# Optimization experiments

Measured on AMD Instinct MI355X. Metric: run time of the kernel, lower is better.

The kernel has to match this reference:

```python
import jax, jax.numpy as jnp
import numpy as np

B, S, D_IN = 2, 2048, 1024
H, D_HEAD = 16, 64  # n_heads, output_dim == hidden_size


def setup_inputs() -> dict:
    key = jax.random.key(0)
    k1, k2, k3 = jax.random.split(key, 3)
    x = jax.random.normal(k1, (B, S, D_IN), dtype=jnp.float32)
    # he_normal-ish init: std = sqrt(2 / fan_in)
    kernel = jax.random.normal(k2, (3, H, D_IN, D_HEAD), dtype=jnp.float32) * np.float32(np.sqrt(2.0 / D_IN))
    WO = jax.random.normal(k3, (1, H * D_HEAD, D_IN), dtype=jnp.float32) * np.float32(np.sqrt(2.0 / (H * D_HEAD)))
    return {"x": x, "kernel": kernel, "WO": WO}


def reference(x, kernel, WO):
    b, s, _ = x.shape
    h, d = kernel.shape[1], kernel.shape[3]
    # K.dot(x, kernel[i]): contract x last axis with kernel axis -2 -> (B,S,H,d);
    # original then permutes to (B,H,S,d); fuse both into one einsum.
    q = jnp.einsum('bsm,hmd->bhsd', x, kernel[0])
    k = jnp.einsum('bsm,hmd->bhsd', x, kernel[1])
    v = jnp.einsum('bsm,hmd->bhsd', x, kernel[2])
    # scores scaled by /output_dim /hidden_size /n_heads (output_dim==hidden_size)
    scale = jnp.float32(1.0 / (d * d * h))
    scores = jnp.einsum('bhsd,bhtd->bhst', q, k) * scale  # (B,H,S,S)
    attn = jax.nn.softmax(scores, axis=-1)
    out = jnp.einsum('bhst,bhtd->bhsd', attn, v)          # (B,H,S,d)
    # original: permute to (B,S,d,H) then reshape to (B,S,d*H) -> d-major, H-minor
    out = jnp.transpose(out, (0, 2, 3, 1)).reshape(b, s, d * h)
    out = jnp.einsum('bsf,fm->bsm', out, WO[0])           # (B,S,D_IN)
    return out
```

## Files before the change

### kernel.cpp

```cpp
#include <hip/hip_runtime.h>
#include <hip/hip_bf16.h>


typedef unsigned short u16;
typedef __attribute__((ext_vector_type(8))) short bf16x8;
typedef __attribute__((ext_vector_type(4))) short bf16x4;
typedef __attribute__((ext_vector_type(4))) float f32x4;
typedef __attribute__((ext_vector_type(4))) unsigned short u16x4;
typedef __attribute__((ext_vector_type(8))) unsigned short u16x8;

#define SCALE 1.52587890625e-05f

__device__ __forceinline__ u16 f2bf(float f) {
  unsigned int u = __float_as_uint(f);
  return (u16)((u + 0x7FFFu + ((u >> 16) & 1u)) >> 16);
}
__device__ __forceinline__ float bf2f(u16 v) {
  return __uint_as_float(((unsigned int)v) << 16);
}

__device__ __forceinline__ f32x4 mfma16(bf16x8 a, bf16x8 b, f32x4 c) {
  return __builtin_amdgcn_mfma_f32_16x16x32_bf16(a, b, c, 0, 0, 0);
}

__device__ __forceinline__ void gl_lds16(const u16* g, u16* l) {
  __builtin_amdgcn_global_load_lds((const __attribute__((address_space(1))) void*)g,
                                   (__attribute__((address_space(3))) void*)l, 16, 0, 0);
}

__global__ void split_f32(const float* __restrict__ x, u16* __restrict__ hi,
                          u16* __restrict__ lo, int n4) {
  int i = blockIdx.x * 256 + threadIdx.x;
  if (i >= n4) return;
  float4 v = ((const float4*)x)[i];
  float vv[4] = {v.x, v.y, v.z, v.w};
  u16x4 h, l;
#pragma unroll
  for (int j = 0; j < 4; ++j) {
    u16 hb = f2bf(vv[j]);
    h[j] = hb;
    l[j] = f2bf(vv[j] - bf2f(hb));
  }
  ((u16x4*)hi)[i] = h;
  ((u16x4*)lo)[i] = l;
}

__global__ void prep_w(const float* __restrict__ w, u16* __restrict__ bhi,
                       u16* __restrict__ blo) {
  __shared__ float t[64 * 65];
  int mt = blockIdx.x, th = blockIdx.y;
  float scl = (th < 16) ? SCALE : 1.0f;
  int tid = threadIdx.x;
  for (int i = 0; i < 16; ++i) {
    int idx = tid + i * 256;
    int ms = idx >> 6, d = idx & 63;
    t[d * 65 + ms] = w[(size_t)(th * 1024 + mt * 64 + ms) * 64 + d];
  }
  __syncthreads();
  for (int i = 0; i < 16; ++i) {
    int idx = tid + i * 256;
    int ds = idx >> 6, mm = idx & 63;
    float v = t[ds * 65 + mm] * scl;
    size_t o = (size_t)(th * 64 + ds) * 1024 + mt * 64 + mm;
    u16 hb = f2bf(v);
    bhi[o] = hb;
    blo[o] = f2bf(v - bf2f(hb));
  }
}

__global__ void prep_wo(const float* __restrict__ wo, u16* __restrict__ bhi,
                        u16* __restrict__ blo) {
  __shared__ float t[64 * 65];
  int mt = blockIdx.x, kt = blockIdx.y;
  int tid = threadIdx.x;
  for (int i = 0; i < 16; ++i) {
    int idx = tid + i * 256;
    int d = idx >> 6, mm = idx & 63;
    t[mm * 65 + d] = wo[(size_t)(d * 16 + kt) * 1024 + mt * 64 + mm];
  }
  __syncthreads();
  for (int i = 0; i < 16; ++i) {
    int idx = tid + i * 256;
    int mr = idx >> 6, dc = idx & 63;
    float v = t[mr * 65 + dc];
    size_t o = (size_t)(mt * 64 + mr) * 1024 + kt * 64 + dc;
    u16 hb = f2bf(v);
    bhi[o] = hb;
    blo[o] = f2bf(v - bf2f(hb));
  }
}

template <int MODE>
__global__ __launch_bounds__(256, 2) void gemm_split(
    const u16* __restrict__ Ah_g, const u16* __restrict__ Al_g,
    const u16* __restrict__ Bh_g, const u16* __restrict__ Bl_g,
    u16* __restrict__ Qb, u16* __restrict__ Kb, u16* __restrict__ Vb,
    float* __restrict__ Cf) {
  __shared__ __align__(16) u16 Ah[128 * 32];
  __shared__ __align__(16) u16 Al[128 * 32];
  __shared__ __align__(16) u16 Bh[128 * 32];
  __shared__ __align__(16) u16 Bl[128 * 32];
  int tid = threadIdx.x;
  int lane = tid & 63;
  int l15 = lane & 15, g = lane >> 4;
  int wv = tid >> 6, wm = wv >> 1, wn = wv & 1;
  int m0 = blockIdx.x * 128, n0 = blockIdx.y * 128;

  f32x4 acc[4][4];
#pragma unroll
  for (int i = 0; i < 4; ++i)
#pragma unroll
    for (int j = 0; j < 4; ++j) acc[i][j] = (f32x4){0.f, 0.f, 0.f, 0.f};

  int c0 = tid, c1 = tid + 256;
  int r0 = c0 >> 2, o0 = (c0 & 3) * 8;
  int r1 = c1 >> 2, o1 = (c1 & 3) * 8;
  int wb0 = (tid & 192) * 8, wb1 = ((tid & 192) + 256) * 8;

  for (int kk = 0; kk < 32; ++kk) {
    int k0 = kk * 32;
    __syncthreads();
    gl_lds16(Ah_g + (size_t)(m0 + r0) * 1024 + k0 + o0, &Ah[wb0]);
    gl_lds16(Ah_g + (size_t)(m0 + r1) * 1024 + k0 + o1, &Ah[wb1]);
    gl_lds16(Al_g + (size_t)(m0 + r0) * 1024 + k0 + o0, &Al[wb0]);
    gl_lds16(Al_g + (size_t)(m0 + r1) * 1024 + k0 + o1, &Al[wb1]);
    gl_lds16(Bh_g + (size_t)(n0 + r0) * 1024 + k0 + o0, &Bh[wb0]);
    gl_lds16(Bh_g + (size_t)(n0 + r1) * 1024 + k0 + o1, &Bh[wb1]);
    gl_lds16(Bl_g + (size_t)(n0 + r0) * 1024 + k0 + o0, &Bl[wb0]);
    gl_lds16(Bl_g + (size_t)(n0 + r1) * 1024 + k0 + o1, &Bl[wb1]);
    __syncthreads();

    bf16x8 fa_h[4], fa_l[4], fb_h[4], fb_l[4];
#pragma unroll
    for (int mi = 0; mi < 4; ++mi) {
      int off = (wm * 64 + mi * 16 + l15) * 64 + g * 16;
      fa_h[mi] = *(const bf16x8*)((const char*)Ah + off);
      fa_l[mi] = *(const bf16x8*)((const char*)Al + off);
    }
#pragma unroll
    for (int ni = 0; ni < 4; ++ni) {
      int off = (wn * 64 + ni * 16 + l15) * 64 + g * 16;
      fb_h[ni] = *(const bf16x8*)((const char*)Bh + off);
      fb_l[ni] = *(const bf16x8*)((const char*)Bl + off);
    }
#pragma unroll
    for (int mi = 0; mi < 4; ++mi)
#pragma unroll
      for (int ni = 0; ni < 4; ++ni) {
        acc[mi][ni] = mfma16(fa_h[mi], fb_h[ni], acc[mi][ni]);
        acc[mi][ni] = mfma16(fa_h[mi], fb_l[ni], acc[mi][ni]);
        acc[mi][ni] = mfma16(fa_l[mi], fb_h[ni], acc[mi][ni]);
      }
  }

#pragma unroll
  for (int mi = 0; mi < 4; ++mi)
#pragma unroll
    for (int ni = 0; ni < 4; ++ni)
#pragma unroll
      for (int r = 0; r < 4; ++r) {
        int m = m0 + wm * 64 + mi * 16 + g * 4 + r;
        int n = n0 + wn * 64 + ni * 16 + l15;
        float v = acc[mi][ni][r];
        if (MODE == 0) {
          int th = n >> 6, d = n & 63;
          int t = th >> 4, h = th & 15;
          int b = m >> 11, s = m & 2047;
          if (t == 0)
            Qb[(size_t)((b * 16 + h) * 2048 + s) * 64 + d] = f2bf(v);
          else if (t == 1)
            Kb[(size_t)((b * 16 + h) * 2048 + s) * 64 + d] = f2bf(v);
          else
            Vb[(size_t)((b * 16 + h) * 64 + d) * 2048 + s] = f2bf(v);
        } else {
          Cf[(size_t)m * 1024 + n] = v;
        }
      }
}

__global__ void colsum_v(const u16* __restrict__ Vt, float* __restrict__ cs) {
  int bh = blockIdx.x, tid = threadIdx.x;
  int d = tid >> 2, q = tid & 3;
  const u16x8* row = (const u16x8*)(Vt + (size_t)(bh * 64 + d) * 2048 + q * 512);
  float s = 0.f;
  for (int i = 0; i < 64; ++i) {
    u16x8 v = row[i];
#pragma unroll
    for (int j = 0; j < 8; ++j) s += bf2f(v[j]);
  }
  s += __shfl_xor(s, 1);
  s += __shfl_xor(s, 2);
  if (q == 0) cs[bh * 64 + d] = s;
}

__global__ __launch_bounds__(256, 2) void attn(
    const u16* __restrict__ Qb, const u16* __restrict__ Kb,
    const u16* __restrict__ Vt, const float* __restrict__ csum,
    u16* __restrict__ AOhi, u16* __restrict__ AOlo) {
  __shared__ __align__(16) u16 Kl[2][128 * 64];
  __shared__ __align__(16) u16 Vl[2][64 * 128];
  int swz = (blockIdx.x & 7) * 64 + (blockIdx.x >> 3);
  int qt = swz & 15, bh = swz >> 4;
  int tid = threadIdx.x, lane = tid & 63, w = tid >> 6;
  int l15 = lane & 15, g = lane >> 4;
  const u16* Qg = Qb + (size_t)bh * 2048 * 64;
  const u16* Kg = Kb + (size_t)bh * 2048 * 64;
  const u16* Vg = Vt + (size_t)bh * 64 * 2048;
  int q_base = qt * 128 + w * 32;
  int wbase = tid & 192;

  bf16x8 qf[2][2];
#pragma unroll
  for (int q2 = 0; q2 < 2; ++q2)
#pragma unroll
    for (int ds = 0; ds < 2; ++ds)
      qf[q2][ds] = *(const bf16x8*)(Qg + (size_t)(q_base + q2 * 16 + l15) * 64 +
                                    ds * 32 + g * 8);

  f32x4 acc_e[2][4];
#pragma unroll
  for (int i = 0; i < 4; ++i) {
    acc_e[0][i] = (f32x4){0.f, 0.f, 0.f, 0.f};
    acc_e[1][i] = (f32x4){0.f, 0.f, 0.f, 0.f};
  }
  float lsum[2] = {0.f, 0.f};

  auto STAGE = [&](int buf, int tt0) {
    int t0 = tt0 * 128;
#pragma unroll
    for (int i = 0; i < 4; ++i) {
      int c = tid + i * 256;
      int krow = c >> 3, kblk = c & 7;
      gl_lds16(Kg + (size_t)(t0 + krow) * 64 + ((kblk ^ (krow & 7)) * 8),
               &Kl[buf][(wbase + i * 256) * 8]);
      int vd = c >> 4, vsb = c & 15;
      gl_lds16(Vg + (size_t)vd * 2048 + t0 + ((vsb ^ (vd & 7)) * 8),
               &Vl[buf][(wbase + i * 256) * 8]);
    }
  };

  STAGE(0, 0);

  for (int tt0 = 0; tt0 < 16; ++tt0) {
    int cur = tt0 & 1;
    __syncthreads();
    if (tt0 + 1 < 16) STAGE(cur ^ 1, tt0 + 1);

    const char* Kc = (const char*)&Kl[cur][0];
    const char* Vc = (const char*)&Vl[cur][0];

    f32x4 sc[2][8];
#pragma unroll
    for (int tt = 0; tt < 8; ++tt) {
      sc[0][tt] = (f32x4){0.f, 0.f, 0.f, 0.f};
      sc[1][tt] = (f32x4){0.f, 0.f, 0.f, 0.f};
    }
#pragma unroll
    for (int tt = 0; tt < 8; ++tt)
#pragma unroll
      for (int ds = 0; ds < 2; ++ds) {
        int row = tt * 16 + l15;
        int off = row * 128 + ((((ds * 4 + g) ^ (row & 7)) << 4));
        bf16x8 kf = *(const bf16x8*)(Kc + off);
        sc[0][tt] = mfma16(kf, qf[0][ds], sc[0][tt]);
        sc[1][tt] = mfma16(kf, qf[1][ds], sc[1][tt]);
      }

    bf16x8 pe[2][4];
#pragma unroll
    for (int q2 = 0; q2 < 2; ++q2)
#pragma unroll
      for (int ks = 0; ks < 4; ++ks)
#pragma unroll
        for (int blk = 0; blk < 2; ++blk)
#pragma unroll
          for (int r = 0; r < 4; ++r) {
            float e = __expf(sc[q2][ks * 2 + blk][r]) - 1.0f;
            lsum[q2] += e;
            pe[q2][ks][blk * 4 + r] = (short)(__float_as_uint(e) >> 16);
          }

    int xm = (l15 & 7) << 4;
    const char* Vrow = Vc + l15 * 256;
#pragma unroll
    for (int ks = 0; ks < 4; ++ks) {
      int t0a = (ks * 64 + 8 * g) ^ xm;
      int t1a = (ks * 64 + 32 + 8 * g) ^ xm;
#pragma unroll
      for (int dt = 0; dt < 4; ++dt) {
        bf16x4 lo = *(const bf16x4*)(Vrow + dt * 4096 + t0a);
        bf16x4 hi = *(const bf16x4*)(Vrow + dt * 4096 + t1a);
        bf16x8 vf = (bf16x8){lo[0], lo[1], lo[2], lo[3],
                             hi[0], hi[1], hi[2], hi[3]};
        acc_e[0][dt] = mfma16(pe[0][ks], vf, acc_e[0][dt]);
        acc_e[1][dt] = mfma16(pe[1][ks], vf, acc_e[1][dt]);
      }
    }
  }

  float lt[2];
#pragma unroll
  for (int q2 = 0; q2 < 2; ++q2) {
    float v = lsum[q2];
    v += __shfl_xor(v, 16);
    v += __shfl_xor(v, 32);
    lt[q2] = 2048.0f + v;
  }
  float linv[2][4];
#pragma unroll
  for (int q2 = 0; q2 < 2; ++q2)
#pragma unroll
    for (int r = 0; r < 4; ++r) linv[q2][r] = 1.0f / __shfl(lt[q2], g * 4 + r);

  int b = bh >> 4, h = bh & 15;
#pragma unroll
  for (int q2 = 0; q2 < 2; ++q2)
#pragma unroll
    for (int dt = 0; dt < 4; ++dt) {
      float cv = csum[bh * 64 + dt * 16 + l15];
#pragma unroll
      for (int r = 0; r < 4; ++r) {
        int s = q_base + q2 * 16 + g * 4 + r;
        int d = dt * 16 + l15;
        float o = (cv + acc_e[q2][dt][r]) * linv[q2][r];
        u16 hv = f2bf(o);
        size_t ao = ((size_t)(b * 2048 + s) * 16 + h) * 64 + d;
        AOhi[ao] = hv;
        AOlo[ao] = f2bf(o - bf2f(hv));
      }
    }
}

extern "C" void kernel_launch(void* const* d_in, const int* in_sizes, int n_in,
                              void* d_out, int out_size, void* d_ws,
                              size_t ws_size, hipStream_t stream) {
  const float* x = (const float*)d_in[0];
  const float* krn = (const float*)d_in[1];
  const float* wo = (const float*)d_in[2];
  float* out = (float*)d_out;

  u16* p = (u16*)d_ws;
  u16* Xhi = p;   p += 4096 * 1024;
  u16* Xlo = p;   p += 4096 * 1024;
  u16* Wthi = p;  p += 3072 * 1024;
  u16* Wtlo = p;  p += 3072 * 1024;
  u16* WOthi = p; p += 1024 * 1024;
  u16* WOtlo = p; p += 1024 * 1024;
  u16* Qb = p;    p += 4194304;
  u16* Kb = p;    p += 4194304;
  u16* Vtb = p;   p += 4194304;
  u16* AOhi = p;  p += 4194304;
  u16* AOlo = p;  p += 4194304;
  float* Csum = (float*)p;

  split_f32<<<4096, 256, 0, stream>>>(x, Xhi, Xlo, 1048576);
  prep_w<<<dim3(16, 48), 256, 0, stream>>>(krn, Wthi, Wtlo);
  prep_wo<<<dim3(16, 16), 256, 0, stream>>>(wo, WOthi, WOtlo);
  gemm_split<0><<<dim3(32, 24), 256, 0, stream>>>(Xhi, Xlo, Wthi, Wtlo, Qb, Kb,
                                                  Vtb, nullptr);
  colsum_v<<<32, 256, 0, stream>>>(Vtb, Csum);
  attn<<<512, 256, 0, stream>>>(Qb, Kb, Vtb, Csum, AOhi, AOlo);
  gemm_split<1><<<dim3(32, 8), 256, 0, stream>>>(AOhi, AOlo, WOthi, WOtlo,
                                                 nullptr, nullptr, nullptr, out);
}
```

Before: 259.7 us.

## Double-buffer GEMM tiles, use exp2 with folded log2e, MFMA row sums, wider colsum

The split-bf16 GEMM now double-buffers its LDS tiles, issuing the next k-slice load before computing the current one so global loads overlap MFMA work. In attention, log2(e) is folded into the Q weight scale so exp2f replaces __expf, the bf16 truncation uses a byte-perm instead of per-element shifts, and the softmax row sums come from an MFMA against a ones vector instead of scalar adds plus shuffles. colsum_v is spread over 8x more blocks so it uses more of the GPU. The row sums now add up the bf16-truncated probabilities rather than the fp32 values, which slightly changes numerics, and doubling the GEMM LDS footprint may affect occupancy.

```diff
diff --git a/kernel.cpp b/kernel.cpp
--- a/kernel.cpp
+++ b/kernel.cpp
@@ -8,6 +8,7 @@
 typedef __attribute__((ext_vector_type(4))) float f32x4;
 typedef __attribute__((ext_vector_type(4))) unsigned short u16x4;
 typedef __attribute__((ext_vector_type(8))) unsigned short u16x8;
+typedef __attribute__((ext_vector_type(4))) unsigned int u32x4;
 
 #define SCALE 1.52587890625e-05f
 
@@ -49,7 +50,7 @@
                        u16* __restrict__ blo) {
   __shared__ float t[64 * 65];
   int mt = blockIdx.x, th = blockIdx.y;
-  float scl = (th < 16) ? SCALE : 1.0f;
+  float scl = (th < 16) ? SCALE * 1.4426950408889634f : 1.0f;
   int tid = threadIdx.x;
   for (int i = 0; i < 16; ++i) {
     int idx = tid + i * 256;
@@ -96,10 +97,10 @@
     const u16* __restrict__ Bh_g, const u16* __restrict__ Bl_g,
     u16* __restrict__ Qb, u16* __restrict__ Kb, u16* __restrict__ Vb,
     float* __restrict__ Cf) {
-  __shared__ __align__(16) u16 Ah[128 * 32];
-  __shared__ __align__(16) u16 Al[128 * 32];
-  __shared__ __align__(16) u16 Bh[128 * 32];
-  __shared__ __align__(16) u16 Bl[128 * 32];
+  __shared__ __align__(16) u16 Ah[2][128 * 32];
+  __shared__ __align__(16) u16 Al[2][128 * 32];
+  __shared__ __align__(16) u16 Bh[2][128 * 32];
+  __shared__ __align__(16) u16 Bl[2][128 * 32];
   int tid = threadIdx.x;
   int lane = tid & 63;
   int l15 = lane & 15, g = lane >> 4;
@@ -117,31 +118,37 @@
   int r1 = c1 >> 2, o1 = (c1 & 3) * 8;
   int wb0 = (tid & 192) * 8, wb1 = ((tid & 192) + 256) * 8;
 
+  auto STAGE = [&](int buf, int kk) {
+    int k0 = kk * 32;
+    gl_lds16(Ah_g + (size_t)(m0 + r0) * 1024 + k0 + o0, &Ah[buf][wb0]);
+    gl_lds16(Ah_g + (size_t)(m0 + r1) * 1024 + k0 + o1, &Ah[buf][wb1]);
+    gl_lds16(Al_g + (size_t)(m0 + r0) * 1024 + k0 + o0, &Al[buf][wb0]);
+    gl_lds16(Al_g + (size_t)(m0 + r1) * 1024 + k0 + o1, &Al[buf][wb1]);
+    gl_lds16(Bh_g + (size_t)(n0 + r0) * 1024 + k0 + o0, &Bh[buf][wb0]);
+    gl_lds16(Bh_g + (size_t)(n0 + r1) * 1024 + k0 + o1, &Bh[buf][wb1]);
+    gl_lds16(Bl_g + (size_t)(n0 + r0) * 1024 + k0 + o0, &Bl[buf][wb0]);
+    gl_lds16(Bl_g + (size_t)(n0 + r1) * 1024 + k0 + o1, &Bl[buf][wb1]);
+  };
+
+  STAGE(0, 0);
+
   for (int kk = 0; kk < 32; ++kk) {
-    int k0 = kk * 32;
+    int cur = kk & 1;
     __syncthreads();
-    gl_lds16(Ah_g + (size_t)(m0 + r0) * 1024 + k0 + o0, &Ah[wb0]);
-    gl_lds16(Ah_g + (size_t)(m0 + r1) * 1024 + k0 + o1, &Ah[wb1]);
-    gl_lds16(Al_g + (size_t)(m0 + r0) * 1024 + k0 + o0, &Al[wb0]);
-    gl_lds16(Al_g + (size_t)(m0 + r1) * 1024 + k0 + o1, &Al[wb1]);
-    gl_lds16(Bh_g + (size_t)(n0 + r0) * 1024 + k0 + o0, &Bh[wb0]);
-    gl_lds16(Bh_g + (size_t)(n0 + r1) * 1024 + k0 + o1, &Bh[wb1]);
-    gl_lds16(Bl_g + (size_t)(n0 + r0) * 1024 + k0 + o0, &Bl[wb0]);
-    gl_lds16(Bl_g + (size_t)(n0 + r1) * 1024 + k0 + o1, &Bl[wb1]);
-    __syncthreads();
+    if (kk + 1 < 32) STAGE(cur ^ 1, kk + 1);
 
     bf16x8 fa_h[4], fa_l[4], fb_h[4], fb_l[4];
 #pragma unroll
     for (int mi = 0; mi < 4; ++mi) {
       int off = (wm * 64 + mi * 16 + l15) * 64 + g * 16;
-      fa_h[mi] = *(const bf16x8*)((const char*)Ah + off);
-      fa_l[mi] = *(const bf16x8*)((const char*)Al + off);
+      fa_h[mi] = *(const bf16x8*)((const char*)&Ah[cur][0] + off);
+      fa_l[mi] = *(const bf16x8*)((const char*)&Al[cur][0] + off);
     }
 #pragma unroll
     for (int ni = 0; ni < 4; ++ni) {
       int off = (wn * 64 + ni * 16 + l15) * 64 + g * 16;
-      fb_h[ni] = *(const bf16x8*)((const char*)Bh + off);
-      fb_l[ni] = *(const bf16x8*)((const char*)Bl + off);
+      fb_h[ni] = *(const bf16x8*)((const char*)&Bh[cur][0] + off);
+      fb_l[ni] = *(const bf16x8*)((const char*)&Bl[cur][0] + off);
     }
 #pragma unroll
     for (int mi = 0; mi < 4; ++mi)
@@ -179,18 +186,25 @@
 }
 
 __global__ void colsum_v(const u16* __restrict__ Vt, float* __restrict__ cs) {
-  int bh = blockIdx.x, tid = threadIdx.x;
-  int d = tid >> 2, q = tid & 3;
-  const u16x8* row = (const u16x8*)(Vt + (size_t)(bh * 64 + d) * 2048 + q * 512);
+  int blk = blockIdx.x;
+  int bh = blk >> 3, dg = blk & 7;
+  int tid = threadIdx.x;
+  int ld = tid >> 5, l32 = tid & 31;
+  int d = dg * 8 + ld;
+  const u16x8* row = (const u16x8*)(Vt + (size_t)(bh * 64 + d) * 2048);
   float s = 0.f;
-  for (int i = 0; i < 64; ++i) {
-    u16x8 v = row[i];
+#pragma unroll
+  for (int i = 0; i < 8; ++i) {
+    u16x8 v = row[l32 + i * 32];
 #pragma unroll
     for (int j = 0; j < 8; ++j) s += bf2f(v[j]);
   }
   s += __shfl_xor(s, 1);
   s += __shfl_xor(s, 2);
-  if (q == 0) cs[bh * 64 + d] = s;
+  s += __shfl_xor(s, 4);
+  s += __shfl_xor(s, 8);
+  s += __shfl_xor(s, 16);
+  if (l32 == 0) cs[bh * 64 + d] = s;
 }
 
 __global__ __launch_bounds__(256, 2) void attn(
@@ -217,13 +231,17 @@
       qf[q2][ds] = *(const bf16x8*)(Qg + (size_t)(q_base + q2 * 16 + l15) * 64 +
                                     ds * 32 + g * 8);
 
-  f32x4 acc_e[2][4];
+  f32x4 acc_e[2][4], acc_l[2];
 #pragma unroll
   for (int i = 0; i < 4; ++i) {
     acc_e[0][i] = (f32x4){0.f, 0.f, 0.f, 0.f};
     acc_e[1][i] = (f32x4){0.f, 0.f, 0.f, 0.f};
   }
-  float lsum[2] = {0.f, 0.f};
+  acc_l[0] = (f32x4){0.f, 0.f, 0.f, 0.f};
+  acc_l[1] = (f32x4){0.f, 0.f, 0.f, 0.f};
+  bf16x8 ones;
+#pragma unroll
+  for (int j = 0; j < 8; ++j) ones[j] = (short)0x3F80;
 
   auto STAGE = [&](int buf, int tt0) {
     int t0 = tt0 * 128;
@@ -241,6 +259,8 @@
 
   STAGE(0, 0);
 
+  union PU { u32x4 u; bf16x8 b; };
+
   for (int tt0 = 0; tt0 < 16; ++tt0) {
     int cur = tt0 & 1;
     __syncthreads();
@@ -266,19 +286,25 @@
         sc[1][tt] = mfma16(kf, qf[1][ds], sc[1][tt]);
       }
 
-    bf16x8 pe[2][4];
+    PU pe[2][4];
 #pragma unroll
     for (int q2 = 0; q2 < 2; ++q2)
 #pragma unroll
-      for (int ks = 0; ks < 4; ++ks)
-#pragma unroll
-        for (int blk = 0; blk < 2; ++blk)
-#pragma unroll
-          for (int r = 0; r < 4; ++r) {
-            float e = __expf(sc[q2][ks * 2 + blk][r]) - 1.0f;
-            lsum[q2] += e;
-            pe[q2][ks][blk * 4 + r] = (short)(__float_as_uint(e) >> 16);
-          }
+      for (int ks = 0; ks < 4; ++ks) {
+#pragma unroll
+        for (int blk = 0; blk < 2; ++blk) {
+          f32x4 s4 = sc[q2][ks * 2 + blk];
+          float e0 = exp2f(s4[0]) - 1.0f;
+          float e1 = exp2f(s4[1]) - 1.0f;
+          float e2 = exp2f(s4[2]) - 1.0f;
+          float e3 = exp2f(s4[3]) - 1.0f;
+          pe[q2][ks].u[blk * 2] = __builtin_amdgcn_perm(
+              __float_as_uint(e1), __float_as_uint(e0), 0x07060302u);
+          pe[q2][ks].u[blk * 2 + 1] = __builtin_amdgcn_perm(
+              __float_as_uint(e3), __float_as_uint(e2), 0x07060302u);
+        }
+        acc_l[q2] = mfma16(pe[q2][ks].b, ones, acc_l[q2]);
+      }
 
     int xm = (l15 & 7) << 4;
     const char* Vrow = Vc + l15 * 256;
@@ -292,25 +318,18 @@
         bf16x4 hi = *(const bf16x4*)(Vrow + dt * 4096 + t1a);
         bf16x8 vf = (bf16x8){lo[0], lo[1], lo[2], lo[3],
                              hi[0], hi[1], hi[2], hi[3]};
-        acc_e[0][dt] = mfma16(pe[0][ks], vf, acc_e[0][dt]);
-        acc_e[1][dt] = mfma16(pe[1][ks], vf, acc_e[1][dt]);
-      }
-    }
-  }
-
-  float lt[2];
-#pragma unroll
-  for (int q2 = 0; q2 < 2; ++q2) {
-    float v = lsum[q2];
-    v += __shfl_xor(v, 16);
-    v += __shfl_xor(v, 32);
-    lt[q2] = 2048.0f + v;
-  }
+        acc_e[0][dt] = mfma16(pe[0][ks].b, vf, acc_e[0][dt]);
+        acc_e[1][dt] = mfma16(pe[1][ks].b, vf, acc_e[1][dt]);
+      }
+    }
+  }
+
   float linv[2][4];
 #pragma unroll
   for (int q2 = 0; q2 < 2; ++q2)
 #pragma unroll
-    for (int r = 0; r < 4; ++r) linv[q2][r] = 1.0f / __shfl(lt[q2], g * 4 + r);
+    for (int r = 0; r < 4; ++r)
+      linv[q2][r] = 1.0f / (2048.0f + acc_l[q2][r]);
 
   int b = bh >> 4, h = bh & 15;
 #pragma unroll
@@ -358,7 +377,7 @@
   prep_wo<<<dim3(16, 16), 256, 0, stream>>>(wo, WOthi, WOtlo);
   gemm_split<0><<<dim3(32, 24), 256, 0, stream>>>(Xhi, Xlo, Wthi, Wtlo, Qb, Kb,
                                                   Vtb, nullptr);
-  colsum_v<<<32, 256, 0, stream>>>(Vtb, Csum);
+  colsum_v<<<256, 256, 0, stream>>>(Vtb, Csum);
   attn<<<512, 256, 0, stream>>>(Qb, Kb, Vtb, Csum, AOhi, AOlo);
   gemm_split<1><<<dim3(32, 8), 256, 0, stream>>>(AOhi, AOlo, WOthi, WOtlo,
                                                  nullptr, nullptr, nullptr, out);
```

Result: slower. 295.9 us (+13.9%).
